# Optimization experiments

Hardware: AMD Instinct MI355X
Metric: run time of the kernel (lower is better)

Reference implementation:

```python
import jax, jax.numpy as jnp
import numpy as np
from jax import lax

RATIOS = [0.5, 1.0, 2.0]
SCALES = [8, 16, 32]
BASE = 16
FEAT_STRIDE = 16
NMS_THRESH = 0.7
PRE_NMS = 2000
POST_NMS = 300
MIN_SIZE = 16.0
SCALE = 1.0
A = len(RATIOS) * len(SCALES)  # 9


def _anchor_base():
    ab = []
    py = px = BASE / 2.0
    for r in RATIOS:
        for s in SCALES:
            h = BASE * s * np.sqrt(r)
            w = BASE * s * np.sqrt(1.0 / r)
            ab.append([py - h / 2.0, px - w / 2.0, py + h / 2.0, px + w / 2.0])
    return jnp.asarray(np.array(ab, dtype=np.float32))  # (A,4)


def _shifted_anchors(H, W):
    base = _anchor_base()
    sy = jnp.arange(H, dtype=jnp.float32) * FEAT_STRIDE
    sx = jnp.arange(W, dtype=jnp.float32) * FEAT_STRIDE
    gy, gx = jnp.meshgrid(sy, sx, indexing='ij')
    shift = jnp.stack([gy.ravel(), gx.ravel(), gy.ravel(), gx.ravel()], axis=1)  # (K,4)
    return (shift[:, None, :] + base[None, :, :]).reshape(-1, 4)  # (K*A,4)


def _conv(x, w, b, pad):
    y = lax.conv_general_dilated(x, w, (1, 1), ((pad, pad), (pad, pad)),
                                 dimension_numbers=('NCHW', 'OIHW', 'NCHW'))
    return y + b[None, :, None, None]


def _loc2bbox(anchor, loc):
    h = anchor[:, 2] - anchor[:, 0]
    w = anchor[:, 3] - anchor[:, 1]
    cy = anchor[:, 0] + 0.5 * h
    cx = anchor[:, 1] + 0.5 * w
    dy, dx, dh, dw = loc[:, 0], loc[:, 1], loc[:, 2], loc[:, 3]
    ncy = dy * h + cy
    ncx = dx * w + cx
    nh = jnp.exp(dh) * h
    nw = jnp.exp(dw) * w
    return jnp.stack([ncy - 0.5 * nh, ncx - 0.5 * nw, ncy + 0.5 * nh, ncx + 0.5 * nw], axis=1)


def _iou_matrix(b):
    area = (b[:, 2] - b[:, 0]) * (b[:, 3] - b[:, 1])
    ty = jnp.maximum(b[:, None, 0], b[None, :, 0])
    tx = jnp.maximum(b[:, None, 1], b[None, :, 1])
    by = jnp.minimum(b[:, None, 2], b[None, :, 2])
    bx = jnp.minimum(b[:, None, 3], b[None, :, 3])
    inter = jnp.maximum(by - ty, 0.0) * jnp.maximum(bx - tx, 0.0)
    return inter / (area[:, None] + area[None, :] - inter)


def _proposals(loc_i, fg_i, anchor, img_h, img_w):
    boxes = _loc2bbox(anchor, loc_i)
    boxes = jnp.stack([
        jnp.clip(boxes[:, 0], 0.0, float(img_h)),
        jnp.clip(boxes[:, 1], 0.0, float(img_w)),
        jnp.clip(boxes[:, 2], 0.0, float(img_h)),
        jnp.clip(boxes[:, 3], 0.0, float(img_w)),
    ], axis=1)
    hs = boxes[:, 2] - boxes[:, 0]
    ws = boxes[:, 3] - boxes[:, 1]
    valid = (hs >= MIN_SIZE * SCALE) & (ws >= MIN_SIZE * SCALE)
    sc = jnp.where(valid, fg_i, -jnp.inf)
    top_sc, idx = lax.top_k(sc, PRE_NMS)          # sorted by score desc
    b = boxes[idx]                                # (PRE_NMS,4)
    iou = _iou_matrix(b)                          # (PRE_NMS,PRE_NMS)
    rng = jnp.arange(PRE_NMS)

    def body(i, keep):
        sup = (iou[i] > NMS_THRESH) & keep[i] & (rng > i)
        return keep & ~sup

    keep = lax.fori_loop(0, PRE_NMS, body, top_sc > -jnp.inf)
    order = jnp.argsort(jnp.where(keep, rng, PRE_NMS))  # kept indices first, score order
    sel = order[:POST_NMS]
    n_keep = jnp.sum(keep)
    valid_out = jnp.arange(POST_NMS) < n_keep
    rois = jnp.where(valid_out[:, None], b[sel], 0.0)
    return rois, valid_out


def setup_inputs() -> dict:
    key = jax.random.key(0)
    ks = jax.random.split(key, 4)
    return {
        'x': jax.random.normal(ks[0], (4, 1024, 64, 64), dtype=jnp.float32),
        'conv1_w': 0.01 * jax.random.normal(ks[1], (512, 1024, 3, 3), dtype=jnp.float32),
        'conv1_b': jnp.zeros((512,), dtype=jnp.float32),
        'score_w': 0.01 * jax.random.normal(ks[2], (18, 512, 1, 1), dtype=jnp.float32),
        'score_b': jnp.zeros((18,), dtype=jnp.float32),
        'loc_w': 0.01 * jax.random.normal(ks[3], (36, 512, 1, 1), dtype=jnp.float32),
        'loc_b': jnp.zeros((36,), dtype=jnp.float32),
        'img_h': 1024,
        'img_w': 1024,
    }


def reference(x, conv1_w, conv1_b, score_w, score_b, loc_w, loc_b, img_h, img_w):
    n, _, H, W = x.shape
    anchor = _shifted_anchors(H, W)                       # (HWA,4)
    mid = jax.nn.relu(_conv(x, conv1_w, conv1_b, 1))
    rpn_locs = _conv(mid, loc_w, loc_b, 0).transpose(0, 2, 3, 1).reshape(n, -1, 4)
    rpn_scores = _conv(mid, score_w, score_b, 0).transpose(0, 2, 3, 1)
    soft = jax.nn.softmax(rpn_scores.reshape(n, H, W, A, 2), axis=4)
    rpn_fg = soft[..., 1].reshape(n, -1)
    rpn_scores = rpn_scores.reshape(n, -1, 2)
    rois, valid = jax.vmap(lambda l, s: _proposals(l, s, anchor, img_h, img_w))(rpn_locs, rpn_fg)
    roi_indices = jnp.where(valid, jnp.arange(n, dtype=jnp.int32)[:, None], -1)
    return (rpn_locs, rpn_scores, rois.reshape(-1, 4), roi_indices.reshape(-1), anchor)
```

## Files before the change

kernel.cpp:

```cpp
#include <hip/hip_runtime.h>
#include <math.h>

#define NIMG 4
#define CIN 1024
#define CMID 512
#define HGT 64
#define WID 64
#define NA 9
#define NPOS 36864
#define PRE 2000
#define POST 300

#define LOCOFF   0
#define SCOREOFF 589824
#define ROISOFF  884736
#define RIDXOFF  889536
#define ANCHOFF  890736

__global__ __launch_bounds__(256) void conv1_kernel(
    const float* __restrict__ x, const float* __restrict__ w,
    const float* __restrict__ bias, float* __restrict__ mid)
{
    __shared__ __align__(16) float xs[8][6][68];
    __shared__ __align__(16) float wsh[8][9][32];
    const int t = threadIdx.x;
    const int rowgrp = blockIdx.x, coutgrp = blockIdx.y, img = blockIdx.z;
    const int r0 = rowgrp * 4, c0 = coutgrp * 32;
    const int pixgrp = t & 7, cgrp = (t >> 3) & 7, rowi = t >> 6;
    const int p0 = pixgrp * 8, cc0 = cgrp * 4;

    double acc[8][4];
#pragma unroll
    for (int i = 0; i < 8; ++i)
#pragma unroll
        for (int c = 0; c < 4; ++c) acc[i][c] = 0.0;

    for (int ci0 = 0; ci0 < CIN; ci0 += 8) {
        for (int idx = t; idx < 8 * 6 * 66; idx += 256) {
            int cin = idx / 396, rem = idx % 396;
            int row = rem / 66, col = rem % 66;
            int gr = r0 - 1 + row, gc = col - 1;
            float v = 0.f;
            if (gr >= 0 && gr < HGT && gc >= 0 && gc < WID)
                v = x[((img * CIN + ci0 + cin) * HGT + gr) * WID + gc];
            xs[cin][row][col] = v;
        }
        for (int idx = t; idx < 32 * 72; idx += 256) {
            int cout = idx / 72, r = idx % 72;
            int cin = r / 9, tap = r % 9;
            wsh[cin][tap][cout] = w[(c0 + cout) * (CIN * 9) + (ci0 + cin) * 9 + tap];
        }
        __syncthreads();

#pragma unroll 1
        for (int cin = 0; cin < 8; ++cin) {
#pragma unroll
            for (int dy = 0; dy < 3; ++dy) {
                const float* xr = &xs[cin][rowi + dy][p0];
                float4 xa = *(const float4*)xr;
                float4 xb = *(const float4*)(xr + 4);
                float2 xc = *(const float2*)(xr + 8);
                double xd[10];
                xd[0] = xa.x; xd[1] = xa.y; xd[2] = xa.z; xd[3] = xa.w;
                xd[4] = xb.x; xd[5] = xb.y; xd[6] = xb.z; xd[7] = xb.w;
                xd[8] = xc.x; xd[9] = xc.y;
#pragma unroll
                for (int dx = 0; dx < 3; ++dx) {
                    float4 wv = *(const float4*)(&wsh[cin][dy * 3 + dx][cc0]);
                    double w0 = wv.x, w1 = wv.y, w2 = wv.z, w3 = wv.w;
#pragma unroll
                    for (int i = 0; i < 8; ++i) {
                        double xv = xd[i + dx];
                        acc[i][0] += xv * w0;
                        acc[i][1] += xv * w1;
                        acc[i][2] += xv * w2;
                        acc[i][3] += xv * w3;
                    }
                }
            }
        }
        __syncthreads();
    }

#pragma unroll
    for (int co = 0; co < 4; ++co) {
        double bb = (double)bias[c0 + cc0 + co];
        float tmp[8];
#pragma unroll
        for (int i = 0; i < 8; ++i) {
            double v = acc[i][co] + bb;
            v = v > 0.0 ? v : 0.0;
            tmp[i] = (float)v;
        }
        float* dst = &mid[((img * CMID + c0 + cc0 + co) * HGT + (r0 + rowi)) * WID + p0];
        *(float4*)dst = make_float4(tmp[0], tmp[1], tmp[2], tmp[3]);
        *(float4*)(dst + 4) = make_float4(tmp[4], tmp[5], tmp[6], tmp[7]);
    }
}

__global__ __launch_bounds__(256) void conv1x1_kernel(
    const float* __restrict__ mid,
    const float* __restrict__ sw, const float* __restrict__ sb,
    const float* __restrict__ lw, const float* __restrict__ lb,
    float* __restrict__ out, double* __restrict__ locws, double* __restrict__ keyws)
{
    const int t = threadIdx.x;
    const int p = blockIdx.x * 256 + t;
    const int g = blockIdx.y;
    const int img = blockIdx.z;

    double acc[14];
#pragma unroll
    for (int k = 0; k < 14; ++k) acc[k] = 0.0;

    const float* mp = &mid[(size_t)img * CMID * 4096 + p];
    for (int cin = 0; cin < CMID; ++cin) {
        double xd = (double)mp[(size_t)cin * 4096];
#pragma unroll
        for (int k = 0; k < 14; ++k) {
            int c = g * 14 + k;
            double wv = 0.0;
            if (c < 36)      wv = (double)lw[c * CMID + cin];
            else if (c < 54) wv = (double)sw[(c - 36) * CMID + cin];
            acc[k] += xd * wv;
        }
    }

    double prev = 0.0;
#pragma unroll
    for (int k = 0; k < 14; ++k) {
        int c = g * 14 + k;
        if (c >= 54) continue;
        if (c < 36) {
            double v = acc[k] + (double)lb[c];
            int a = c >> 2, cc = c & 3;
            size_t ix = (size_t)img * NPOS + (size_t)p * NA + a;
            locws[ix * 4 + cc] = v;
            out[LOCOFF + ix * 4 + cc] = (float)v;
        } else {
            int sc = c - 36;
            double v = acc[k] + (double)sb[sc];
            int a = sc >> 1;
            size_t ix = (size_t)img * NPOS + (size_t)p * NA + a;
            out[SCOREOFF + ix * 2 + (sc & 1)] = (float)v;
            if (sc & 1) keyws[ix] = v - prev;
            prev = v;
        }
    }
}

__device__ __forceinline__ unsigned mono_of(double k) {
    unsigned fb = __float_as_uint((float)k);
    return (fb & 0x80000000u) ? ~fb : (fb | 0x80000000u);
}

__global__ __launch_bounds__(256) void boxes_kernel(
    double* __restrict__ keyio, const double* __restrict__ locws,
    const int* __restrict__ imh, const int* __restrict__ imw,
    float* __restrict__ out, double* __restrict__ boxes, unsigned* __restrict__ hist)
{
    __shared__ unsigned lh[4096];
    const int t = threadIdx.x;
    const int img = blockIdx.y;
    const int pos = blockIdx.x * 256 + t;
    for (int i = t; i < 4096; i += 256) lh[i] = 0;
    __syncthreads();

    int a = pos % 9, hw = pos / 9;
    int hy = hw >> 6, hx = hw & 63;
    int r_idx = a / 3, s_idx = a % 3;
    double ratio = r_idx == 0 ? 0.5 : (r_idx == 1 ? 1.0 : 2.0);
    double scl   = s_idx == 0 ? 8.0 : (s_idx == 1 ? 16.0 : 32.0);
    double hh2 = 8.0 * scl * sqrt(ratio);
    double ww2 = 8.0 * scl * sqrt(1.0 / ratio);
    float ay1 = (float)(8.0 - hh2), ax1 = (float)(8.0 - ww2);
    float ay2 = (float)(8.0 + hh2), ax2 = (float)(8.0 + ww2);
    float sy = (float)(hy * 16), sx = (float)(hx * 16);
    float A0 = sy + ay1, A1 = sx + ax1, A2 = sy + ay2, A3 = sx + ax2;
    if (img == 0) {
        size_t ao = ANCHOFF + (size_t)pos * 4;
        out[ao + 0] = A0; out[ao + 1] = A1; out[ao + 2] = A2; out[ao + 3] = A3;
    }

    size_t ix = (size_t)img * NPOS + pos;
    const double* lp = &locws[ix * 4];
    double h = (double)A2 - (double)A0, w_ = (double)A3 - (double)A1;
    double cy = (double)A0 + 0.5 * h, cx = (double)A1 + 0.5 * w_;
    double dy = lp[0], dx = lp[1], dh = lp[2], dw = lp[3];
    double ncy = dy * h + cy, ncx = dx * w_ + cx;
    double nh = exp(dh) * h, nw = exp(dw) * w_;
    double Hc = (double)imh[0], Wc = (double)imw[0];
    double y1 = ncy - 0.5 * nh, x1 = ncx - 0.5 * nw;
    double y2 = ncy + 0.5 * nh, x2 = ncx + 0.5 * nw;
    y1 = fmin(fmax(y1, 0.0), Hc); x1 = fmin(fmax(x1, 0.0), Wc);
    y2 = fmin(fmax(y2, 0.0), Hc); x2 = fmin(fmax(x2, 0.0), Wc);
    boxes[ix * 4 + 0] = y1; boxes[ix * 4 + 1] = x1;
    boxes[ix * 4 + 2] = y2; boxes[ix * 4 + 3] = x2;

    bool valid = ((y2 - y1) >= 16.0) && ((x2 - x1) >= 16.0);
    double kg = valid ? keyio[ix] : -INFINITY;
    keyio[ix] = kg;
    atomicAdd(&lh[mono_of(kg) >> 20], 1u);
    __syncthreads();
    for (int i = t; i < 4096; i += 256)
        if (lh[i]) atomicAdd(&hist[img * 4096 + i], lh[i]);
}

__global__ void cutoff_kernel(const unsigned* __restrict__ hist, int* __restrict__ cutoffb)
{
    if (threadIdx.x) return;
    int img = blockIdx.x;
    unsigned cum = 0; int cb = 0;
    for (int b = 4095; b >= 0; --b) {
        cum += hist[img * 4096 + b];
        if (cum >= PRE) { cb = b; break; }
    }
    cutoffb[img] = cb;
}

__global__ __launch_bounds__(256) void compact_kernel(
    const double* __restrict__ keyio, const int* __restrict__ cutoffb,
    int* __restrict__ candCnt, int* __restrict__ candIdx, double* __restrict__ candKey)
{
    int img = blockIdx.y;
    int pos = blockIdx.x * 256 + threadIdx.x;
    size_t ix = (size_t)img * NPOS + pos;
    double k = keyio[ix];
    if ((int)(mono_of(k) >> 20) >= cutoffb[img]) {
        int p = atomicAdd(&candCnt[img], 1);
        candIdx[img * NPOS + p] = pos;
        candKey[(size_t)img * NPOS + p] = k;
    }
}

__global__ __launch_bounds__(256) void rank_kernel(
    const int* __restrict__ candCnt, const int* __restrict__ candIdx,
    const double* __restrict__ candKey, const double* __restrict__ boxes,
    int* __restrict__ topIdx, int* __restrict__ topValid, double* __restrict__ bsel)
{
    __shared__ double sk[256];
    __shared__ int si[256];
    int img = blockIdx.y, t = threadIdx.x;
    int M = candCnt[img];
    if (blockIdx.x * 256 >= M) return;
    int i = blockIdx.x * 256 + t;
    bool act = i < M;
    double ki = 0.0; int pi = 0;
    if (act) { ki = candKey[(size_t)img * NPOS + i]; pi = candIdx[img * NPOS + i]; }
    int rank = 0;
    for (int jb = 0; jb < M; jb += 256) {
        int j = jb + t;
        if (j < M) { sk[t] = candKey[(size_t)img * NPOS + j]; si[t] = candIdx[img * NPOS + j]; }
        __syncthreads();
        int lim = min(256, M - jb);
        if (act) {
            for (int jj = 0; jj < lim; ++jj) {
                double kj = sk[jj]; int pj = si[jj];
                rank += (kj > ki || (kj == ki && pj < pi)) ? 1 : 0;
            }
        }
        __syncthreads();
    }
    if (act && rank < PRE) {
        topIdx[img * PRE + rank] = pi;
        topValid[img * PRE + rank] = (ki != -INFINITY) ? 1 : 0;
        const double* bp = &boxes[((size_t)img * NPOS + pi) * 4];
        double* bs = &bsel[((size_t)img * PRE + rank) * 4];
        bs[0] = bp[0]; bs[1] = bp[1]; bs[2] = bp[2]; bs[3] = bp[3];
    }
}

__global__ __launch_bounds__(256) void mask_kernel(
    const double* __restrict__ bsel, unsigned long long* __restrict__ mask)
{
    int i = blockIdx.x, img = blockIdx.y, t = threadIdx.x;
    const double* bi = &bsel[((size_t)img * PRE + i) * 4];
    double y1i = bi[0], x1i = bi[1], y2i = bi[2], x2i = bi[3];
    double ai = (y2i - y1i) * (x2i - x1i);
#pragma unroll 1
    for (int it = 0; it < 8; ++it) {
        int j = it * 256 + t;
        bool pred = false;
        if (j < PRE && j > i) {
            const double* bj = &bsel[((size_t)img * PRE + j) * 4];
            double ty = fmax(y1i, bj[0]), tx = fmax(x1i, bj[1]);
            double by = fmin(y2i, bj[2]), bx = fmin(x2i, bj[3]);
            double inter = fmax(by - ty, 0.0) * fmax(bx - tx, 0.0);
            double aj = (bj[2] - bj[0]) * (bj[3] - bj[1]);
            double iou = inter / (ai + aj - inter);
            pred = iou > 0.7;
        }
        unsigned long long m = __ballot(pred);
        if ((t & 63) == 0)
            mask[((size_t)img * PRE + i) * 32 + it * 4 + (t >> 6)] = m;
    }
}

__global__ void nms_kernel(const unsigned long long* __restrict__ mask,
                           const int* __restrict__ topValid, int* __restrict__ keepA)
{
    int img = blockIdx.x, lane = threadIdx.x;
    size_t base = (size_t)img * PRE;
    unsigned long long remv = 0;
    if (lane < 32) {
        unsigned long long tv = 0;
        for (int b = 0; b < 64; ++b) {
            int idx = lane * 64 + b;
            if (idx < PRE && topValid[base + idx]) tv |= (1ull << b);
        }
        remv = ~tv;
    }
    const unsigned long long* mrow = &mask[base * 32];
    unsigned long long c0 = 0, c1 = 0, c2 = 0, c3 = 0;
    if (lane < 32) {
        c0 = mrow[(size_t)0 * 32 + lane]; c1 = mrow[(size_t)1 * 32 + lane];
        c2 = mrow[(size_t)2 * 32 + lane]; c3 = mrow[(size_t)3 * 32 + lane];
    }
    for (int i = 0; i < PRE; i += 4) {
        unsigned long long n0 = 0, n1 = 0, n2 = 0, n3 = 0;
        if (lane < 32 && i + 4 < PRE) {
            n0 = mrow[(size_t)(i + 4) * 32 + lane];
            n1 = mrow[(size_t)(i + 5) * 32 + lane];
            n2 = mrow[(size_t)(i + 6) * 32 + lane];
            n3 = mrow[(size_t)(i + 7) * 32 + lane];
        }
        {
            unsigned long long rw = __shfl(remv, i >> 6);
            int kp = !((rw >> (i & 63)) & 1ull);
            if (lane == 0) keepA[base + i] = kp;
            if (kp) remv |= c0;
        }
        {
            int ii = i + 1;
            unsigned long long rw = __shfl(remv, ii >> 6);
            int kp = !((rw >> (ii & 63)) & 1ull);
            if (lane == 0) keepA[base + ii] = kp;
            if (kp) remv |= c1;
        }
        {
            int ii = i + 2;
            unsigned long long rw = __shfl(remv, ii >> 6);
            int kp = !((rw >> (ii & 63)) & 1ull);
            if (lane == 0) keepA[base + ii] = kp;
            if (kp) remv |= c2;
        }
        {
            int ii = i + 3;
            unsigned long long rw = __shfl(remv, ii >> 6);
            int kp = !((rw >> (ii & 63)) & 1ull);
            if (lane == 0) keepA[base + ii] = kp;
            if (kp) remv |= c3;
        }
        c0 = n0; c1 = n1; c2 = n2; c3 = n3;
    }
}

__global__ __launch_bounds__(256) void final_kernel(
    const int* __restrict__ keepA, const double* __restrict__ bsel, float* __restrict__ out)
{
    __shared__ int ssum[256];
    __shared__ int stot;
    int img = blockIdx.x, t = threadIdx.x;
    size_t base = (size_t)img * PRE;
    int loc[8]; int s = 0;
#pragma unroll
    for (int k = 0; k < 8; ++k) {
        int i = t * 8 + k;
        loc[k] = (i < PRE) ? keepA[base + i] : 0;
        s += loc[k];
    }
    ssum[t] = s;
    __syncthreads();
    if (t == 0) {
        int run = 0;
        for (int u = 0; u < 256; ++u) { int tmp = ssum[u]; ssum[u] = run; run += tmp; }
        stot = run;
    }
    __syncthreads();
    int run = ssum[t];
#pragma unroll
    for (int k = 0; k < 8; ++k) {
        int i = t * 8 + k;
        if (i < PRE && loc[k]) {
            int p = run++;
            if (p < POST) {
                const double* bp = &bsel[(base + i) * 4];
                size_t ro = ROISOFF + ((size_t)img * POST + p) * 4;
                out[ro + 0] = (float)bp[0]; out[ro + 1] = (float)bp[1];
                out[ro + 2] = (float)bp[2]; out[ro + 3] = (float)bp[3];
                out[RIDXOFF + img * POST + p] = (float)img;
            }
        }
    }
    __syncthreads();
    int nk = stot;
    for (int r = t; r < POST; r += 256) {
        if (r >= nk) {
            size_t ro = ROISOFF + ((size_t)img * POST + r) * 4;
            out[ro + 0] = 0.f; out[ro + 1] = 0.f; out[ro + 2] = 0.f; out[ro + 3] = 0.f;
            out[RIDXOFF + img * POST + r] = -1.f;
        }
    }
}

extern "C" void kernel_launch(void* const* d_in, const int* in_sizes, int n_in,
                              void* d_out, int out_size, void* d_ws, size_t ws_size,
                              hipStream_t stream)
{
    const float* x   = (const float*)d_in[0];
    const float* c1w = (const float*)d_in[1];
    const float* c1b = (const float*)d_in[2];
    const float* sw  = (const float*)d_in[3];
    const float* sb  = (const float*)d_in[4];
    const float* lw  = (const float*)d_in[5];
    const float* lb  = (const float*)d_in[6];
    const int*   ih  = (const int*)d_in[7];
    const int*   iw  = (const int*)d_in[8];
    float* out = (float*)d_out;
    (void)in_sizes; (void)n_in; (void)out_size; (void)ws_size;

    char* ws = (char*)d_ws;
    size_t off = 0;
    auto alloc = [&](size_t bytes) -> void* {
        void* p = (void*)(ws + off);
        off = (off + bytes + 255) & ~(size_t)255;
        return p;
    };
    float*  mid      = (float*) alloc((size_t)NIMG * CMID * 4096 * 4);
    double* locws    = (double*)alloc((size_t)NIMG * NPOS * 4 * 8);
    double* keyws    = (double*)alloc((size_t)NIMG * NPOS * 8);
    double* boxes    = (double*)alloc((size_t)NIMG * NPOS * 4 * 8);
    unsigned* hist   = (unsigned*)alloc((size_t)NIMG * 4096 * 4);
    int*    cutoffb  = (int*)   alloc(64);
    int*    candCnt  = (int*)   alloc(64);
    int*    candIdx  = (int*)   alloc((size_t)NIMG * NPOS * 4);
    double* candKey  = (double*)alloc((size_t)NIMG * NPOS * 8);
    int*    topIdx   = (int*)   alloc((size_t)NIMG * PRE * 4);
    int*    topValid = (int*)   alloc((size_t)NIMG * PRE * 4);
    double* bsel     = (double*)alloc((size_t)NIMG * PRE * 4 * 8);
    unsigned long long* mask = (unsigned long long*)alloc((size_t)NIMG * PRE * 32 * 8);
    int*    keepA    = (int*)   alloc((size_t)NIMG * PRE * 4);

    hipMemsetAsync(hist, 0, (size_t)NIMG * 4096 * 4, stream);
    hipMemsetAsync(candCnt, 0, 64, stream);

    conv1_kernel  <<<dim3(16, 16, NIMG), 256, 0, stream>>>(x, c1w, c1b, mid);
    conv1x1_kernel<<<dim3(16, 4, NIMG),  256, 0, stream>>>(mid, sw, sb, lw, lb, out, locws, keyws);
    boxes_kernel  <<<dim3(144, NIMG),    256, 0, stream>>>(keyws, locws, ih, iw, out, boxes, hist);
    cutoff_kernel <<<NIMG, 64, 0, stream>>>(hist, cutoffb);
    compact_kernel<<<dim3(144, NIMG),    256, 0, stream>>>(keyws, cutoffb, candCnt, candIdx, candKey);
    rank_kernel   <<<dim3(144, NIMG),    256, 0, stream>>>(candCnt, candIdx, candKey, boxes,
                                                           topIdx, topValid, bsel);
    mask_kernel   <<<dim3(PRE, NIMG),    256, 0, stream>>>(bsel, mask);
    nms_kernel    <<<NIMG, 64, 0, stream>>>(mask, topValid, keepA);
    final_kernel  <<<NIMG, 256, 0, stream>>>(keepA, bsel, out);
}
```

Baseline: 4.993 ms.

## Pre-transpose conv weights and stage conv1 tiles as doubles in LDS

Adds a transpose kernel that reorders the 3x3 conv weights to [cin*tap][cout], so conv1 weight loads are coalesced along output channels. conv1 now stores input and weight tiles as doubles in shared memory, which removes the float-to-double conversions from the inner FMA loop. The input-channel chunk drops from 8 to 4 to keep shared memory size about the same. This doubles the number of sync and load rounds and doubles LDS bandwidth per element, and it adds one extra kernel launch plus a workspace buffer.

Measured after the change: 4.748 ms. 1.05x faster.

```diff
diff --git a/kernel.cpp b/kernel.cpp
--- a/kernel.cpp
+++ b/kernel.cpp
@@ -17,12 +17,34 @@
 #define RIDXOFF  889536
 #define ANCHOFF  890736
 
+__global__ __launch_bounds__(256) void wtrans_kernel(
+    const float* __restrict__ w, float* __restrict__ wt)
+{
+    __shared__ float ts[64][65];
+    const int t = threadIdx.x;
+    const int rt0 = blockIdx.x * 64;
+    const int ct0 = blockIdx.y * 64;
+    const int j = t & 63;
+    const int i0 = t >> 6;
+#pragma unroll
+    for (int k = 0; k < 16; ++k) {
+        int i = i0 + k * 4;
+        ts[i][j] = w[(size_t)(ct0 + i) * (CIN * 9) + rt0 + j];
+    }
+    __syncthreads();
+#pragma unroll
+    for (int k = 0; k < 16; ++k) {
+        int jj = i0 + k * 4;
+        wt[(size_t)(rt0 + jj) * CMID + ct0 + j] = ts[j][jj];
+    }
+}
+
 __global__ __launch_bounds__(256) void conv1_kernel(
-    const float* __restrict__ x, const float* __restrict__ w,
+    const float* __restrict__ x, const float* __restrict__ wt,
     const float* __restrict__ bias, float* __restrict__ mid)
 {
-    __shared__ __align__(16) float xs[8][6][68];
-    __shared__ __align__(16) float wsh[8][9][32];
+    __shared__ __align__(16) double xs[4][6][68];
+    __shared__ __align__(16) double wsh[4][9][32];
     const int t = threadIdx.x;
     const int rowgrp = blockIdx.x, coutgrp = blockIdx.y, img = blockIdx.z;
     const int r0 = rowgrp * 4, c0 = coutgrp * 32;
@@ -35,46 +57,49 @@
 #pragma unroll
         for (int c = 0; c < 4; ++c) acc[i][c] = 0.0;
 
-    for (int ci0 = 0; ci0 < CIN; ci0 += 8) {
-        for (int idx = t; idx < 8 * 6 * 66; idx += 256) {
+    for (int ci0 = 0; ci0 < CIN; ci0 += 4) {
+        for (int idx = t; idx < 4 * 6 * 66; idx += 256) {
             int cin = idx / 396, rem = idx % 396;
             int row = rem / 66, col = rem % 66;
             int gr = r0 - 1 + row, gc = col - 1;
             float v = 0.f;
             if (gr >= 0 && gr < HGT && gc >= 0 && gc < WID)
                 v = x[((img * CIN + ci0 + cin) * HGT + gr) * WID + gc];
-            xs[cin][row][col] = v;
-        }
-        for (int idx = t; idx < 32 * 72; idx += 256) {
-            int cout = idx / 72, r = idx % 72;
-            int cin = r / 9, tap = r % 9;
-            wsh[cin][tap][cout] = w[(c0 + cout) * (CIN * 9) + (ci0 + cin) * 9 + tap];
+            xs[cin][row][col] = (double)v;
+        }
+        for (int idx = t; idx < 4 * 9 * 32; idx += 256) {
+            int cout = idx & 31, r = idx >> 5;
+            wsh[r / 9][r % 9][cout] =
+                (double)wt[(size_t)((ci0 + r / 9) * 9 + r % 9) * CMID + c0 + cout];
         }
         __syncthreads();
 
 #pragma unroll 1
-        for (int cin = 0; cin < 8; ++cin) {
+        for (int cin = 0; cin < 4; ++cin) {
 #pragma unroll
             for (int dy = 0; dy < 3; ++dy) {
-                const float* xr = &xs[cin][rowi + dy][p0];
-                float4 xa = *(const float4*)xr;
-                float4 xb = *(const float4*)(xr + 4);
-                float2 xc = *(const float2*)(xr + 8);
+                const double* xr = &xs[cin][rowi + dy][p0];
+                double2 a0 = *(const double2*)(xr);
+                double2 a1 = *(const double2*)(xr + 2);
+                double2 a2 = *(const double2*)(xr + 4);
+                double2 a3 = *(const double2*)(xr + 6);
+                double2 a4 = *(const double2*)(xr + 8);
                 double xd[10];
-                xd[0] = xa.x; xd[1] = xa.y; xd[2] = xa.z; xd[3] = xa.w;
-                xd[4] = xb.x; xd[5] = xb.y; xd[6] = xb.z; xd[7] = xb.w;
-                xd[8] = xc.x; xd[9] = xc.y;
+                xd[0] = a0.x; xd[1] = a0.y; xd[2] = a1.x; xd[3] = a1.y;
+                xd[4] = a2.x; xd[5] = a2.y; xd[6] = a3.x; xd[7] = a3.y;
+                xd[8] = a4.x; xd[9] = a4.y;
 #pragma unroll
                 for (int dx = 0; dx < 3; ++dx) {
-                    float4 wv = *(const float4*)(&wsh[cin][dy * 3 + dx][cc0]);
-                    double w0 = wv.x, w1 = wv.y, w2 = wv.z, w3 = wv.w;
+                    const double* wp = &wsh[cin][dy * 3 + dx][cc0];
+                    double2 wa = *(const double2*)(wp);
+                    double2 wb = *(const double2*)(wp + 2);
 #pragma unroll
                     for (int i = 0; i < 8; ++i) {
                         double xv = xd[i + dx];
-                        acc[i][0] += xv * w0;
-                        acc[i][1] += xv * w1;
-                        acc[i][2] += xv * w2;
-                        acc[i][3] += xv * w3;
+                        acc[i][0] += xv * wa.x;
+                        acc[i][1] += xv * wa.y;
+                        acc[i][2] += xv * wb.x;
+                        acc[i][3] += xv * wb.y;
                     }
                 }
             }
@@ -427,6 +452,7 @@
         return p;
     };
     float*  mid      = (float*) alloc((size_t)NIMG * CMID * 4096 * 4);
+    float*  wtr      = (float*) alloc((size_t)CMID * CIN * 9 * 4);
     double* locws    = (double*)alloc((size_t)NIMG * NPOS * 4 * 8);
     double* keyws    = (double*)alloc((size_t)NIMG * NPOS * 8);
     double* boxes    = (double*)alloc((size_t)NIMG * NPOS * 4 * 8);
@@ -444,7 +470,8 @@
     hipMemsetAsync(hist, 0, (size_t)NIMG * 4096 * 4, stream);
     hipMemsetAsync(candCnt, 0, 64, stream);
 
-    conv1_kernel  <<<dim3(16, 16, NIMG), 256, 0, stream>>>(x, c1w, c1b, mid);
+    wtrans_kernel <<<dim3(144, 8),       256, 0, stream>>>(c1w, wtr);
+    conv1_kernel  <<<dim3(16, 16, NIMG), 256, 0, stream>>>(x, wtr, c1b, mid);
     conv1x1_kernel<<<dim3(16, 4, NIMG),  256, 0, stream>>>(mid, sw, sb, lw, lb, out, locws, keyws);
     boxes_kernel  <<<dim3(144, NIMG),    256, 0, stream>>>(keyws, locws, ih, iw, out, boxes, hist);
     cutoff_kernel <<<NIMG, 64, 0, stream>>>(hist, cutoffb);
```
